# Optimization experiments

Measured on AMD Instinct MI355X. Metric: run time of the kernel, lower is better.

The kernel has to match this reference:

```python
import jax, jax.numpy as jnp
import numpy as np
from jax import lax

M = 4194304      # total ray samples
N_RAYS = 16384   # number of rays
INTERVAL = 0.5
ALPHA_INIT = 1e-6


def setup_inputs() -> dict:
    key = jax.random.key(0)
    k1, k2, k3 = jax.random.split(key, 3)
    density = jax.random.normal(k1, (M,), dtype=jnp.float32)
    rgb_raw = jax.random.normal(k2, (M, 3), dtype=jnp.float32)
    # act_shift buffer: log(1/(1-alpha_init) - 1)
    shift = jnp.full((1,), np.log(1.0 / (1.0 - ALPHA_INIT) - 1.0), dtype=jnp.float32)
    ray_id = jnp.sort(jax.random.randint(k3, (M,), 0, N_RAYS, dtype=jnp.int32))
    return {"density": density, "rgb_raw": rgb_raw, "shift": shift,
            "ray_id": ray_id, "N": N_RAYS}


def _seg_comb(a, b):
    # associative operator for segmented product scan: (prod, reset_flag)
    pa, fa = a
    pb, fb = b
    return jnp.where(fb, pb, pa * pb), fa | fb


def reference(density, rgb_raw, shift, ray_id, N):
    # Raw2Alpha: alpha = 1 - exp(-softplus(density + shift) * interval)
    s = jax.nn.softplus(density + shift[0]) * INTERVAL   # [M], >= 0
    alpha = -jnp.expm1(-s)                                # 1 - exp(-s), stable
    om = jnp.exp(-s)                                      # 1 - alpha, exact

    # Alphas2Weights: per-ray transmittance scan over variable-length segments.
    first = jnp.concatenate([jnp.ones((1,), bool), ray_id[1:] != ray_id[:-1]])
    # inclusive segmented cumprod of (1 - alpha)
    Tin, _ = lax.associative_scan(_seg_comb, (om, first))
    # exclusive transmittance: T_i = prod of (1-alpha_j) for j earlier in same ray
    T = jnp.where(first, 1.0, jnp.concatenate([jnp.ones((1,), om.dtype), Tin[:-1]]))
    weights = alpha * T                                   # [M]
    # leftover transmittance per ray (1 for rays with no samples)
    alphainv_last = jax.ops.segment_prod(om, ray_id, num_segments=N)  # [N]

    # alpha compositing of colors against a white background
    rgb = jax.nn.sigmoid(rgb_raw)                          # [M,3]
    rgb_marched = (jax.ops.segment_sum(weights[:, None] * rgb, ray_id, num_segments=N)
                   + alphainv_last[:, None])               # [N,3]
    return rgb_marched
```

## Files before the change

kernel.cpp:

```cpp
#include <hip/hip_runtime.h>
#include <math.h>


__device__ __forceinline__ float sigm(float x) {
    return __builtin_amdgcn_rcpf(1.0f + __expf(-x));
}

template <int Ctrl, int RowMask>
__device__ __forceinline__ float dpp_mul(float x) {
    const int s = __builtin_amdgcn_update_dpp(
        __float_as_int(1.0f), __float_as_int(x), Ctrl, RowMask, 0xf, false);
    return x * __int_as_float(s);
}
template <int Ctrl, int RowMask>
__device__ __forceinline__ float dpp_add(float x) {
    const int s = __builtin_amdgcn_update_dpp(
        __float_as_int(0.0f), __float_as_int(x), Ctrl, RowMask, 0xf, false);
    return x + __int_as_float(s);
}

__device__ __forceinline__ float wave_cumprod(float p) {
    p = dpp_mul<0x111, 0xf>(p);
    p = dpp_mul<0x112, 0xf>(p);
    p = dpp_mul<0x114, 0xf>(p);
    p = dpp_mul<0x118, 0xf>(p);
    p = dpp_mul<0x142, 0xa>(p);
    p = dpp_mul<0x143, 0xc>(p);
    return p;
}
__device__ __forceinline__ float wave_cumsum(float a) {
    a = dpp_add<0x111, 0xf>(a);
    a = dpp_add<0x112, 0xf>(a);
    a = dpp_add<0x114, 0xf>(a);
    a = dpp_add<0x118, 0xf>(a);
    a = dpp_add<0x142, 0xa>(a);
    a = dpp_add<0x143, 0xc>(a);
    return a;
}
__device__ __forceinline__ float lane63(float x) {
    return __int_as_float(__builtin_amdgcn_readlane(__float_as_int(x), 63));
}

__global__ __launch_bounds__(256) void seg_starts_kernel(
    const int* __restrict__ ray_id, int* __restrict__ starts, int M, int N)
{
    const int i4 = (blockIdx.x * 256 + threadIdx.x) * 4;
    if (i4 >= M) return;

    if (i4 + 3 < M) {
        const int4 v = *(const int4*)(ray_id + i4);
        const int prev = (i4 == 0) ? -1 : ray_id[i4 - 1];
        for (int r = prev + 1; r <= v.x; ++r) starts[r] = i4 + 0;
        for (int r = v.x + 1; r <= v.y; ++r) starts[r] = i4 + 1;
        for (int r = v.y + 1; r <= v.z; ++r) starts[r] = i4 + 2;
        for (int r = v.z + 1; r <= v.w; ++r) starts[r] = i4 + 3;
        if (i4 + 4 == M) {
            for (int r = v.w + 1; r <= N; ++r) starts[r] = M;
        }
    } else {
        int prev = (i4 == 0) ? -1 : ray_id[i4 - 1];
        for (int k = 0; k < 4 && i4 + k < M; ++k) {
            const int cur = ray_id[i4 + k];
            for (int r = prev + 1; r <= cur; ++r) starts[r] = i4 + k;
            prev = cur;
            if (i4 + k == M - 1)
                for (int r = cur + 1; r <= N; ++r) starts[r] = M;
        }
    }
}

__global__ __launch_bounds__(256) void voxel_march_kernel(
    const float* __restrict__ density,
    const float* __restrict__ rgb_raw,
    const float* __restrict__ shift,
    const int*   __restrict__ starts,
    float* __restrict__ out,
    int M, int N)
{
    const int lane = threadIdx.x & 63;
    const int wave = threadIdx.x >> 6;
    const int ray  = blockIdx.x * 4 + wave;
    if (ray >= N) return;

    const float sh = shift[0];
    const int begin = starts[ray];
    const int end   = starts[ray + 1];

    float carry = 1.0f;
    float acc0 = 0.0f, acc1 = 0.0f, acc2 = 0.0f;

    for (int base = (begin & ~3); base < end; base += 256) {
        const int b4 = base + 4 * lane;
        const int ba = min(b4, M - 4);

        const float4 dd = *(const float4*)(density + ba);
        const float4* rp = (const float4*)(rgb_raw + 3 * ba);
        const float4 c0 = rp[0], c1 = rp[1], c2 = rp[2];

        const bool v0 = (b4 + 0 >= begin) & (b4 + 0 < end);
        const bool v1 = (b4 + 1 >= begin) & (b4 + 1 < end);
        const bool v2 = (b4 + 2 >= begin) & (b4 + 2 < end);
        const bool v3 = (b4 + 3 >= begin) & (b4 + 3 < end);
        const float d0 = v0 ? dd.x : -1e30f;
        const float d1 = v1 ? dd.y : -1e30f;
        const float d2 = v2 ? dd.z : -1e30f;
        const float d3 = v3 ? dd.w : -1e30f;

        const float om0 = __builtin_amdgcn_rsqf(1.0f + __expf(d0 + sh));
        const float om1 = __builtin_amdgcn_rsqf(1.0f + __expf(d1 + sh));
        const float om2 = __builtin_amdgcn_rsqf(1.0f + __expf(d2 + sh));
        const float om3 = __builtin_amdgcn_rsqf(1.0f + __expf(d3 + sh));
        const float al0 = 1.0f - om0, al1 = 1.0f - om1;
        const float al2 = 1.0f - om2, al3 = 1.0f - om3;

        const float p = wave_cumprod((om0 * om1) * (om2 * om3));

        const float excl = __int_as_float(__builtin_amdgcn_update_dpp(
            __float_as_int(1.0f), __float_as_int(p), 0x138, 0xf, 0xf, false));

        float t = carry * excl;
        const float w0 = al0 * t; t *= om0;
        const float w1 = al1 * t; t *= om1;
        const float w2 = al2 * t; t *= om2;
        const float w3 = al3 * t;

        acc0 += w0 * sigm(c0.x) + w1 * sigm(c0.w) + w2 * sigm(c1.z) + w3 * sigm(c2.y);
        acc1 += w0 * sigm(c0.y) + w1 * sigm(c1.x) + w2 * sigm(c1.w) + w3 * sigm(c2.z);
        acc2 += w0 * sigm(c0.z) + w1 * sigm(c1.y) + w2 * sigm(c2.x) + w3 * sigm(c2.w);

        carry *= lane63(p);
    }

    const float tot0 = lane63(wave_cumsum(acc0));
    const float tot1 = lane63(wave_cumsum(acc1));
    const float tot2 = lane63(wave_cumsum(acc2));

    if (lane == 0) {
        out[3 * ray + 0] = tot0 + carry;
        out[3 * ray + 1] = tot1 + carry;
        out[3 * ray + 2] = tot2 + carry;
    }
}

extern "C" void kernel_launch(void* const* d_in, const int* in_sizes, int n_in,
                              void* d_out, int out_size, void* d_ws, size_t ws_size,
                              hipStream_t stream)
{
    const float* density = (const float*)d_in[0];
    const float* rgb_raw = (const float*)d_in[1];
    const float* shift   = (const float*)d_in[2];
    const int*   ray_id  = (const int*)d_in[3];
    float* out = (float*)d_out;

    const int M = in_sizes[0];
    const int N = out_size / 3;

    int* starts = (int*)d_ws;
    const int t1 = (M + 3) / 4;
    seg_starts_kernel<<<(t1 + 255) / 256, 256, 0, stream>>>(ray_id, starts, M, N);

    const int rays_per_block = 4;
    const int blocks = (N + rays_per_block - 1) / rays_per_block;
    voxel_march_kernel<<<blocks, 256, 0, stream>>>(density, rgb_raw, shift,
                                                   starts, out, M, N);
}
```

Baseline: 111.1 us.

## Fuse segment-start computation into march kernel via wave-parallel binary search

```diff
diff --git a/kernel.cpp b/kernel.cpp
--- a/kernel.cpp
+++ b/kernel.cpp
@@ -41,70 +41,81 @@
     return __int_as_float(__builtin_amdgcn_readlane(__float_as_int(x), 63));
 }
 
-__global__ __launch_bounds__(256) void seg_starts_kernel(
-    const int* __restrict__ ray_id, int* __restrict__ starts, int M, int N)
+__device__ __forceinline__ int wave_lower_bound(const int* __restrict__ a,
+                                                int n, int target, int lane)
 {
-    const int i4 = (blockIdx.x * 256 + threadIdx.x) * 4;
-    if (i4 >= M) return;
-
-    if (i4 + 3 < M) {
-        const int4 v = *(const int4*)(ray_id + i4);
-        const int prev = (i4 == 0) ? -1 : ray_id[i4 - 1];
-        for (int r = prev + 1; r <= v.x; ++r) starts[r] = i4 + 0;
-        for (int r = v.x + 1; r <= v.y; ++r) starts[r] = i4 + 1;
-        for (int r = v.y + 1; r <= v.z; ++r) starts[r] = i4 + 2;
-        for (int r = v.z + 1; r <= v.w; ++r) starts[r] = i4 + 3;
-        if (i4 + 4 == M) {
-            for (int r = v.w + 1; r <= N; ++r) starts[r] = M;
-        }
-    } else {
-        int prev = (i4 == 0) ? -1 : ray_id[i4 - 1];
-        for (int k = 0; k < 4 && i4 + k < M; ++k) {
-            const int cur = ray_id[i4 + k];
-            for (int r = prev + 1; r <= cur; ++r) starts[r] = i4 + k;
-            prev = cur;
-            if (i4 + k == M - 1)
-                for (int r = cur + 1; r <= N; ++r) starts[r] = M;
-        }
+    int lo = 0, hi = n;
+    while (hi - lo > 64) {
+        const int step = ((hi - lo) + 63) >> 6;
+        const int pos  = lo + lane * step;
+        const bool pred = (pos < n) && (a[pos] < target);
+        const int cnt = __popcll(__ballot(pred));
+        if (cnt == 0) break;
+        const int nhi = lo + cnt * step;
+        lo = lo + (cnt - 1) * step + 1;
+        hi = min(hi, nhi);
     }
+    const int pos = lo + lane;
+    const bool pred = (pos < n) && (a[pos] < target);
+    return lo + __popcll(__ballot(pred));
 }
 
-__global__ __launch_bounds__(256) void voxel_march_kernel(
+__global__ __launch_bounds__(256) void fused_march_kernel(
     const float* __restrict__ density,
     const float* __restrict__ rgb_raw,
     const float* __restrict__ shift,
-    const int*   __restrict__ starts,
+    const int*   __restrict__ ray_id,
     float* __restrict__ out,
     int M, int N)
 {
+    __shared__ int bnd[5];
     const int lane = threadIdx.x & 63;
     const int wave = threadIdx.x >> 6;
-    const int ray  = blockIdx.x * 4 + wave;
+    const int r0   = blockIdx.x * 4;
+
+    {
+        const int b = wave_lower_bound(ray_id, M, r0 + wave, lane);
+        if (lane == 0) bnd[wave] = b;
+        if (wave == 0) {
+            const int b4 = wave_lower_bound(ray_id, M, r0 + 4, lane);
+            if (lane == 0) bnd[4] = b4;
+        }
+    }
+    __syncthreads();
+
+    const int ray = r0 + wave;
     if (ray >= N) return;
 
-    const float sh = shift[0];
-    const int begin = starts[ray];
-    const int end   = starts[ray + 1];
+    const float sh   = shift[0];
+    const int begin  = bnd[wave];
+    const int end    = bnd[wave + 1];
 
     float carry = 1.0f;
     float acc0 = 0.0f, acc1 = 0.0f, acc2 = 0.0f;
 
     for (int base = (begin & ~3); base < end; base += 256) {
         const int b4 = base + 4 * lane;
-        const int ba = min(b4, M - 4);
 
-        const float4 dd = *(const float4*)(density + ba);
-        const float4* rp = (const float4*)(rgb_raw + 3 * ba);
-        const float4 c0 = rp[0], c1 = rp[1], c2 = rp[2];
+        float d0 = -1e30f, d1 = -1e30f, d2 = -1e30f, d3 = -1e30f;
+        float4 c0 = {0.f, 0.f, 0.f, 0.f};
+        float4 c1 = {0.f, 0.f, 0.f, 0.f};
+        float4 c2 = {0.f, 0.f, 0.f, 0.f};
 
-        const bool v0 = (b4 + 0 >= begin) & (b4 + 0 < end);
-        const bool v1 = (b4 + 1 >= begin) & (b4 + 1 < end);
-        const bool v2 = (b4 + 2 >= begin) & (b4 + 2 < end);
-        const bool v3 = (b4 + 3 >= begin) & (b4 + 3 < end);
-        const float d0 = v0 ? dd.x : -1e30f;
-        const float d1 = v1 ? dd.y : -1e30f;
-        const float d2 = v2 ? dd.z : -1e30f;
-        const float d3 = v3 ? dd.w : -1e30f;
+        if (b4 < end) {
+            const int ba = min(b4, M - 4);
+            const float4 dd = *(const float4*)(density + ba);
+            const float4* rp = (const float4*)(rgb_raw + 3 * ba);
+            c0 = rp[0]; c1 = rp[1]; c2 = rp[2];
+
+            const bool v0 = (b4 + 0 >= begin);
+            const bool v1 = (b4 + 1 >= begin) & (b4 + 1 < end);
+            const bool v2 = (b4 + 2 >= begin) & (b4 + 2 < end);
+            const bool v3 = (b4 + 3 >= begin) & (b4 + 3 < end);
+            d0 = v0 ? dd.x : -1e30f;
+            d1 = v1 ? dd.y : -1e30f;
+            d2 = v2 ? dd.z : -1e30f;
+            d3 = v3 ? dd.w : -1e30f;
+        }
 
         const float om0 = __builtin_amdgcn_rsqf(1.0f + __expf(d0 + sh));
         const float om1 = __builtin_amdgcn_rsqf(1.0f + __expf(d1 + sh));
@@ -155,12 +166,7 @@
     const int M = in_sizes[0];
     const int N = out_size / 3;
 
-    int* starts = (int*)d_ws;
-    const int t1 = (M + 3) / 4;
-    seg_starts_kernel<<<(t1 + 255) / 256, 256, 0, stream>>>(ray_id, starts, M, N);
-
-    const int rays_per_block = 4;
-    const int blocks = (N + rays_per_block - 1) / rays_per_block;
-    voxel_march_kernel<<<blocks, 256, 0, stream>>>(density, rgb_raw, shift,
-                                                   starts, out, M, N);
+    const int blocks = (N + 3) / 4;
+    fused_march_kernel<<<blocks, 256, 0, stream>>>(density, rgb_raw, shift,
+                                                   ray_id, out, M, N);
 }
```

Result: slower. 114.5 us (+3.0%).

## Switch to one sample per lane with register prefetch of next chunk

Applied to the files above, without the earlier changes.

```diff
diff --git a/kernel.cpp b/kernel.cpp
--- a/kernel.cpp
+++ b/kernel.cpp
@@ -89,46 +89,45 @@
     float carry = 1.0f;
     float acc0 = 0.0f, acc1 = 0.0f, acc2 = 0.0f;
 
-    for (int base = (begin & ~3); base < end; base += 256) {
-        const int b4 = base + 4 * lane;
-        const int ba = min(b4, M - 4);
+    float dcur = -1e30f, c0 = 0.0f, c1 = 0.0f, c2 = 0.0f;
+    if (begin < end) {
+        const int g  = begin + lane;
+        const int gc = min(g, M - 1);
+        dcur = density[gc];
+        c0 = rgb_raw[3 * gc + 0];
+        c1 = rgb_raw[3 * gc + 1];
+        c2 = rgb_raw[3 * gc + 2];
+        if (g >= end) dcur = -1e30f;
+    }
 
-        const float4 dd = *(const float4*)(density + ba);
-        const float4* rp = (const float4*)(rgb_raw + 3 * ba);
-        const float4 c0 = rp[0], c1 = rp[1], c2 = rp[2];
+    for (int base = begin; base < end; base += 64) {
+        float dnx = -1e30f, n0 = 0.0f, n1 = 0.0f, n2 = 0.0f;
+        const int nb = base + 64;
+        if (nb < end) {
+            const int g  = nb + lane;
+            const int gc = min(g, M - 1);
+            dnx = density[gc];
+            n0 = rgb_raw[3 * gc + 0];
+            n1 = rgb_raw[3 * gc + 1];
+            n2 = rgb_raw[3 * gc + 2];
+            if (g >= end) dnx = -1e30f;
+        }
 
-        const bool v0 = (b4 + 0 >= begin) & (b4 + 0 < end);
-        const bool v1 = (b4 + 1 >= begin) & (b4 + 1 < end);
-        const bool v2 = (b4 + 2 >= begin) & (b4 + 2 < end);
-        const bool v3 = (b4 + 3 >= begin) & (b4 + 3 < end);
-        const float d0 = v0 ? dd.x : -1e30f;
-        const float d1 = v1 ? dd.y : -1e30f;
-        const float d2 = v2 ? dd.z : -1e30f;
-        const float d3 = v3 ? dd.w : -1e30f;
+        const float om = __builtin_amdgcn_rsqf(1.0f + __expf(dcur + sh));
+        const float al = 1.0f - om;
 
-        const float om0 = __builtin_amdgcn_rsqf(1.0f + __expf(d0 + sh));
-        const float om1 = __builtin_amdgcn_rsqf(1.0f + __expf(d1 + sh));
-        const float om2 = __builtin_amdgcn_rsqf(1.0f + __expf(d2 + sh));
-        const float om3 = __builtin_amdgcn_rsqf(1.0f + __expf(d3 + sh));
-        const float al0 = 1.0f - om0, al1 = 1.0f - om1;
-        const float al2 = 1.0f - om2, al3 = 1.0f - om3;
-
-        const float p = wave_cumprod((om0 * om1) * (om2 * om3));
-
+        const float p = wave_cumprod(om);
         const float excl = __int_as_float(__builtin_amdgcn_update_dpp(
             __float_as_int(1.0f), __float_as_int(p), 0x138, 0xf, 0xf, false));
 
-        float t = carry * excl;
-        const float w0 = al0 * t; t *= om0;
-        const float w1 = al1 * t; t *= om1;
-        const float w2 = al2 * t; t *= om2;
-        const float w3 = al3 * t;
-
-        acc0 += w0 * sigm(c0.x) + w1 * sigm(c0.w) + w2 * sigm(c1.z) + w3 * sigm(c2.y);
-        acc1 += w0 * sigm(c0.y) + w1 * sigm(c1.x) + w2 * sigm(c1.w) + w3 * sigm(c2.z);
-        acc2 += w0 * sigm(c0.z) + w1 * sigm(c1.y) + w2 * sigm(c2.x) + w3 * sigm(c2.w);
+        const float w = al * (carry * excl);
+        acc0 += w * sigm(c0);
+        acc1 += w * sigm(c1);
+        acc2 += w * sigm(c2);
 
         carry *= lane63(p);
+
+        dcur = dnx; c0 = n0; c1 = n1; c2 = n2;
     }
 
     const float tot0 = lane63(wave_cumsum(acc0));
```

Measured after the change: 113.7 us. 2.4% more time.

## Process two rays per wavefront using half-wave DPP scans

Applied to the files above, without the earlier changes.

```diff
diff --git a/kernel.cpp b/kernel.cpp
--- a/kernel.cpp
+++ b/kernel.cpp
@@ -19,26 +19,24 @@
     return x + __int_as_float(s);
 }
 
-__device__ __forceinline__ float wave_cumprod(float p) {
+__device__ __forceinline__ float half_cumprod(float p) {
     p = dpp_mul<0x111, 0xf>(p);
     p = dpp_mul<0x112, 0xf>(p);
     p = dpp_mul<0x114, 0xf>(p);
     p = dpp_mul<0x118, 0xf>(p);
     p = dpp_mul<0x142, 0xa>(p);
-    p = dpp_mul<0x143, 0xc>(p);
     return p;
 }
-__device__ __forceinline__ float wave_cumsum(float a) {
+__device__ __forceinline__ float half_cumsum(float a) {
     a = dpp_add<0x111, 0xf>(a);
     a = dpp_add<0x112, 0xf>(a);
     a = dpp_add<0x114, 0xf>(a);
     a = dpp_add<0x118, 0xf>(a);
     a = dpp_add<0x142, 0xa>(a);
-    a = dpp_add<0x143, 0xc>(a);
     return a;
 }
-__device__ __forceinline__ float lane63(float x) {
-    return __int_as_float(__builtin_amdgcn_readlane(__float_as_int(x), 63));
+__device__ __forceinline__ float rdlane(float x, int l) {
+    return __int_as_float(__builtin_amdgcn_readlane(__float_as_int(x), l));
 }
 
 __global__ __launch_bounds__(256) void seg_starts_kernel(
@@ -78,19 +76,23 @@
     int M, int N)
 {
     const int lane = threadIdx.x & 63;
+    const int l32  = lane & 31;
     const int wave = threadIdx.x >> 6;
-    const int ray  = blockIdx.x * 4 + wave;
-    if (ray >= N) return;
+    const int ray  = blockIdx.x * 8 + wave * 2 + (lane >> 5);
+    const bool ray_ok = (ray < N);
 
     const float sh = shift[0];
-    const int begin = starts[ray];
-    const int end   = starts[ray + 1];
+    int begin = 0, end = 0;
+    if (ray_ok) {
+        begin = starts[ray];
+        end   = starts[ray + 1];
+    }
 
     float carry = 1.0f;
     float acc0 = 0.0f, acc1 = 0.0f, acc2 = 0.0f;
 
-    for (int base = (begin & ~3); base < end; base += 256) {
-        const int b4 = base + 4 * lane;
+    for (int base = (begin & ~3); base < end; base += 128) {
+        const int b4 = base + 4 * l32;
         const int ba = min(b4, M - 4);
 
         const float4 dd = *(const float4*)(density + ba);
@@ -113,10 +115,11 @@
         const float al0 = 1.0f - om0, al1 = 1.0f - om1;
         const float al2 = 1.0f - om2, al3 = 1.0f - om3;
 
-        const float p = wave_cumprod((om0 * om1) * (om2 * om3));
+        const float p = half_cumprod((om0 * om1) * (om2 * om3));
 
-        const float excl = __int_as_float(__builtin_amdgcn_update_dpp(
+        float excl = __int_as_float(__builtin_amdgcn_update_dpp(
             __float_as_int(1.0f), __float_as_int(p), 0x138, 0xf, 0xf, false));
+        excl = (l32 == 0) ? 1.0f : excl;
 
         float t = carry * excl;
         const float w0 = al0 * t; t *= om0;
@@ -128,17 +131,22 @@
         acc1 += w0 * sigm(c0.y) + w1 * sigm(c1.x) + w2 * sigm(c1.w) + w3 * sigm(c2.z);
         acc2 += w0 * sigm(c0.z) + w1 * sigm(c1.y) + w2 * sigm(c2.x) + w3 * sigm(c2.w);
 
-        carry *= lane63(p);
+        const float cA = rdlane(p, 31);
+        const float cB = rdlane(p, 63);
+        carry *= (lane < 32) ? cA : cB;
     }
 
-    const float tot0 = lane63(wave_cumsum(acc0));
-    const float tot1 = lane63(wave_cumsum(acc1));
-    const float tot2 = lane63(wave_cumsum(acc2));
+    const float s0 = half_cumsum(acc0);
+    const float s1 = half_cumsum(acc1);
+    const float s2 = half_cumsum(acc2);
+    const float t0 = (lane < 32) ? rdlane(s0, 31) : rdlane(s0, 63);
+    const float t1 = (lane < 32) ? rdlane(s1, 31) : rdlane(s1, 63);
+    const float t2 = (lane < 32) ? rdlane(s2, 31) : rdlane(s2, 63);
 
-    if (lane == 0) {
-        out[3 * ray + 0] = tot0 + carry;
-        out[3 * ray + 1] = tot1 + carry;
-        out[3 * ray + 2] = tot2 + carry;
+    if (ray_ok && l32 == 0) {
+        out[3 * ray + 0] = t0 + carry;
+        out[3 * ray + 1] = t1 + carry;
+        out[3 * ray + 2] = t2 + carry;
     }
 }
 
@@ -159,7 +167,7 @@
     const int t1 = (M + 3) / 4;
     seg_starts_kernel<<<(t1 + 255) / 256, 256, 0, stream>>>(ray_id, starts, M, N);
 
-    const int rays_per_block = 4;
+    const int rays_per_block = 8;
     const int blocks = (N + rays_per_block - 1) / rays_per_block;
     voxel_march_kernel<<<blocks, 256, 0, stream>>>(density, rgb_raw, shift,
                                                    starts, out, M, N);
```

Measured after the change: 111.9 us. Within noise of the previous version (+0.7%).
